# Kernel tuning notes

Hardware: AMD Instinct MI355X
Metric: run time of the kernel (lower is better)

## Reference

```python
import jax, jax.numpy as jnp
import numpy as np

# Block node counts (dst nodes are a prefix of src nodes, DGL convention)
N = [540672, 33792, 3072, 512]


def _sage_layer(h, src, dst, num_dst, W_self, W_neigh, b):
    # DGL SAGEConv with 'mean' aggregator:
    #   out = h_dst @ W_self + mean_{u in N(v)} h_u @ W_neigh + b
    msgs = h[src]  # [E, F] ragged gather
    agg = jax.ops.segment_sum(msgs, dst, num_segments=num_dst)
    deg = jax.ops.segment_sum(jnp.ones(dst.shape, h.dtype), dst, num_segments=num_dst)
    mean = agg / jnp.maximum(deg, 1.0)[:, None]
    return h[:num_dst] @ W_self + mean @ W_neigh + b


def setup_inputs() -> dict:
    key = jax.random.key(0)
    ks = jax.random.split(key, 16)
    E = [506880, 30720, 2560]
    in_feats, n_hidden, n_classes = 256, 1024, 47
    sc = lambda f: 1.0 / np.sqrt(f)
    return {
        "x": jax.random.normal(ks[0], (N[0], in_feats), jnp.float32),
        "src0": jax.random.randint(ks[1], (E[0],), 0, N[0]),
        "dst0": jax.random.randint(ks[2], (E[0],), 0, N[1]),
        "src1": jax.random.randint(ks[3], (E[1],), 0, N[1]),
        "dst1": jax.random.randint(ks[4], (E[1],), 0, N[2]),
        "src2": jax.random.randint(ks[5], (E[2],), 0, N[2]),
        "dst2": jax.random.randint(ks[6], (E[2],), 0, N[3]),
        "W_self0": jax.random.normal(ks[7], (in_feats, n_hidden), jnp.float32) * sc(in_feats),
        "W_neigh0": jax.random.normal(ks[8], (in_feats, n_hidden), jnp.float32) * sc(in_feats),
        "b0": jnp.zeros((n_hidden,), jnp.float32),
        "W_self1": jax.random.normal(ks[9], (n_hidden, n_hidden), jnp.float32) * sc(n_hidden),
        "W_neigh1": jax.random.normal(ks[10], (n_hidden, n_hidden), jnp.float32) * sc(n_hidden),
        "b1": jnp.zeros((n_hidden,), jnp.float32),
        "W_self2": jax.random.normal(ks[11], (n_hidden, n_classes), jnp.float32) * sc(n_hidden),
        "W_neigh2": jax.random.normal(ks[12], (n_hidden, n_classes), jnp.float32) * sc(n_hidden),
        "b2": jnp.zeros((n_classes,), jnp.float32),
    }


def reference(x, src0, dst0, src1, dst1, src2, dst2,
              W_self0, W_neigh0, b0, W_self1, W_neigh1, b1,
              W_self2, W_neigh2, b2):
    # Layer 0: [N0, in] -> [N1, hidden], ReLU (dropout omitted: eval mode)
    h = _sage_layer(x, src0, dst0, N[1], W_self0, W_neigh0, b0)
    h = jax.nn.relu(h)
    # Layer 1: [N1, hidden] -> [N2, hidden], ReLU
    h = _sage_layer(h, src1, dst1, N[2], W_self1, W_neigh1, b1)
    h = jax.nn.relu(h)
    # Layer 2: [N2, hidden] -> [N3, classes], no activation
    h = _sage_layer(h, src2, dst2, N[3], W_self2, W_neigh2, b2)
    return h
```

## Files before the change

kernel.cpp:

```cpp
#include <hip/hip_runtime.h>

#define E0 506880
#define E1 30720
#define E2 2560
#define NN0 540672
#define NN1 33792
#define NN2 3072
#define NN3 512
#define F_IN 256
#define F_HID 1024
#define F_OUT 47

typedef __attribute__((ext_vector_type(8))) short short8;
typedef __attribute__((ext_vector_type(4))) float f32x4;

__device__ __forceinline__ float bf_lo(unsigned int u) {
    return __uint_as_float(u << 16);
}
__device__ __forceinline__ float bf_hi(unsigned int u) {
    return __uint_as_float(u & 0xFFFF0000u);
}
__device__ __forceinline__ unsigned short f2bf(float f) {
    unsigned int u = __float_as_uint(f);
    u = (u + 0x7FFFu + ((u >> 16) & 1u)) >> 16;
    return (unsigned short)u;
}
__device__ __forceinline__ unsigned int pack2(float a, float b) {
    return (unsigned int)f2bf(a) | ((unsigned int)f2bf(b) << 16);
}

__global__ __launch_bounds__(256) void count_dst(
    const int* __restrict__ dst, int* __restrict__ cnt, int E)
{
    int i = blockIdx.x * blockDim.x + threadIdx.x;
    if (i < E) atomicAdd(&cnt[dst[i]], 1);
}

__global__ __launch_bounds__(1024) void scan_excl(
    const int* __restrict__ cnt, int* __restrict__ cursor, int n)
{
    __shared__ int part[1024];
    int t = threadIdx.x;
    int per = (n + 1023) >> 10;
    int lo = t * per;
    int hi = min(n, lo + per);
    int s = 0;
    for (int i = lo; i < hi; ++i) s += cnt[i];
    part[t] = s;
    __syncthreads();
    for (int d = 1; d < 1024; d <<= 1) {
        int v = part[t];
        int add = (t >= d) ? part[t - d] : 0;
        __syncthreads();
        part[t] = v + add;
        __syncthreads();
    }
    int off = (t == 0) ? 0 : part[t - 1];
    for (int i = lo; i < hi; ++i) { cursor[i] = off; off += cnt[i]; }
}

__global__ __launch_bounds__(256) void fill_adj(
    const int* __restrict__ src, const int* __restrict__ dst,
    int* __restrict__ cursor, int* __restrict__ adj, int E)
{
    int i = blockIdx.x * blockDim.x + threadIdx.x;
    if (i < E) {
        int pos = atomicAdd(&cursor[dst[i]], 1);
        adj[pos] = src[i];
    }
}

__global__ __launch_bounds__(256) void cast_f32_bf16(
    const float* __restrict__ in, unsigned short* __restrict__ out, int n8)
{
    int i = blockIdx.x * blockDim.x + threadIdx.x;
    if (i >= n8) return;
    float4 a = *(const float4*)(in + (size_t)i * 8);
    float4 b = *(const float4*)(in + (size_t)i * 8 + 4);
    uint4 o;
    o.x = pack2(a.x, a.y); o.y = pack2(a.z, a.w);
    o.z = pack2(b.x, b.y); o.w = pack2(b.z, b.w);
    *(uint4*)(out + (size_t)i * 8) = o;
}

__global__ __launch_bounds__(256) void transpose_cast(
    const float* __restrict__ W, unsigned short* __restrict__ Wt, int K, int N)
{
    __shared__ float t[32][33];
    int k0 = blockIdx.x * 32;
    int n0 = blockIdx.y * 32;
    int tx = threadIdx.x & 31;
    int ty = threadIdx.x >> 5;
    #pragma unroll
    for (int i = 0; i < 4; ++i) {
        int r = ty * 4 + i;
        t[r][tx] = W[(size_t)(k0 + r) * N + n0 + tx];
    }
    __syncthreads();
    #pragma unroll
    for (int i = 0; i < 4; ++i) {
        int nr = ty * 4 + i;
        Wt[(size_t)(n0 + nr) * K + k0 + tx] = f2bf(t[tx][nr]);
    }
}

__global__ __launch_bounds__(256) void gather_mean_f32(
    const float* __restrict__ feat, const int* __restrict__ adj,
    const int* __restrict__ cnt, const int* __restrict__ cur,
    unsigned short* __restrict__ agg, int num_dst)
{
    int wave = (blockIdx.x * blockDim.x + threadIdx.x) >> 6;
    int lane = threadIdx.x & 63;
    if (wave >= num_dst) return;
    int d = cnt[wave];
    int start = cur[wave] - d;
    float4 a0 = make_float4(0.f, 0.f, 0.f, 0.f), a1 = a0, a2 = a0, a3 = a0;
    int j = 0;
    for (; j + 3 < d; j += 4) {
        int i0 = adj[start + j + 0], i1 = adj[start + j + 1];
        int i2 = adj[start + j + 2], i3 = adj[start + j + 3];
        float4 v0 = *(const float4*)(feat + (size_t)i0 * F_IN + lane * 4);
        float4 v1 = *(const float4*)(feat + (size_t)i1 * F_IN + lane * 4);
        float4 v2 = *(const float4*)(feat + (size_t)i2 * F_IN + lane * 4);
        float4 v3 = *(const float4*)(feat + (size_t)i3 * F_IN + lane * 4);
        a0.x += v0.x; a0.y += v0.y; a0.z += v0.z; a0.w += v0.w;
        a1.x += v1.x; a1.y += v1.y; a1.z += v1.z; a1.w += v1.w;
        a2.x += v2.x; a2.y += v2.y; a2.z += v2.z; a2.w += v2.w;
        a3.x += v3.x; a3.y += v3.y; a3.z += v3.z; a3.w += v3.w;
    }
    for (; j < d; ++j) {
        int i0 = adj[start + j];
        float4 v0 = *(const float4*)(feat + (size_t)i0 * F_IN + lane * 4);
        a0.x += v0.x; a0.y += v0.y; a0.z += v0.z; a0.w += v0.w;
    }
    float inv = 1.0f / (float)(d > 0 ? d : 1);
    float sx = (a0.x + a1.x) + (a2.x + a3.x);
    float sy = (a0.y + a1.y) + (a2.y + a3.y);
    float sz = (a0.z + a1.z) + (a2.z + a3.z);
    float sw = (a0.w + a1.w) + (a2.w + a3.w);
    uint2 o;
    o.x = pack2(sx * inv, sy * inv);
    o.y = pack2(sz * inv, sw * inv);
    *(uint2*)(agg + (size_t)wave * F_IN + lane * 4) = o;
}

__global__ __launch_bounds__(256) void gather_mean_bf16(
    const unsigned short* __restrict__ feat, const int* __restrict__ adj,
    const int* __restrict__ cnt, const int* __restrict__ cur,
    unsigned short* __restrict__ agg, int num_dst)
{
    int wave = (blockIdx.x * blockDim.x + threadIdx.x) >> 6;
    int lane = threadIdx.x & 63;
    if (wave >= num_dst) return;
    int d = cnt[wave];
    int start = cur[wave] - d;
    float acc[16];
    #pragma unroll
    for (int c = 0; c < 16; ++c) acc[c] = 0.f;
    int j = 0;
    for (; j + 1 < d; j += 2) {
        const unsigned short* f0 = feat + (size_t)adj[start + j] * F_HID + lane * 16;
        const unsigned short* f1 = feat + (size_t)adj[start + j + 1] * F_HID + lane * 16;
        uint4 p0 = *(const uint4*)f0;
        uint4 p1 = *(const uint4*)(f0 + 8);
        uint4 q0 = *(const uint4*)f1;
        uint4 q1 = *(const uint4*)(f1 + 8);
        acc[0] += bf_lo(p0.x); acc[1] += bf_hi(p0.x);
        acc[2] += bf_lo(p0.y); acc[3] += bf_hi(p0.y);
        acc[4] += bf_lo(p0.z); acc[5] += bf_hi(p0.z);
        acc[6] += bf_lo(p0.w); acc[7] += bf_hi(p0.w);
        acc[8]  += bf_lo(p1.x); acc[9]  += bf_hi(p1.x);
        acc[10] += bf_lo(p1.y); acc[11] += bf_hi(p1.y);
        acc[12] += bf_lo(p1.z); acc[13] += bf_hi(p1.z);
        acc[14] += bf_lo(p1.w); acc[15] += bf_hi(p1.w);
        acc[0] += bf_lo(q0.x); acc[1] += bf_hi(q0.x);
        acc[2] += bf_lo(q0.y); acc[3] += bf_hi(q0.y);
        acc[4] += bf_lo(q0.z); acc[5] += bf_hi(q0.z);
        acc[6] += bf_lo(q0.w); acc[7] += bf_hi(q0.w);
        acc[8]  += bf_lo(q1.x); acc[9]  += bf_hi(q1.x);
        acc[10] += bf_lo(q1.y); acc[11] += bf_hi(q1.y);
        acc[12] += bf_lo(q1.z); acc[13] += bf_hi(q1.z);
        acc[14] += bf_lo(q1.w); acc[15] += bf_hi(q1.w);
    }
    if (j < d) {
        const unsigned short* f0 = feat + (size_t)adj[start + j] * F_HID + lane * 16;
        uint4 p0 = *(const uint4*)f0;
        uint4 p1 = *(const uint4*)(f0 + 8);
        acc[0] += bf_lo(p0.x); acc[1] += bf_hi(p0.x);
        acc[2] += bf_lo(p0.y); acc[3] += bf_hi(p0.y);
        acc[4] += bf_lo(p0.z); acc[5] += bf_hi(p0.z);
        acc[6] += bf_lo(p0.w); acc[7] += bf_hi(p0.w);
        acc[8]  += bf_lo(p1.x); acc[9]  += bf_hi(p1.x);
        acc[10] += bf_lo(p1.y); acc[11] += bf_hi(p1.y);
        acc[12] += bf_lo(p1.z); acc[13] += bf_hi(p1.z);
        acc[14] += bf_lo(p1.w); acc[15] += bf_hi(p1.w);
    }
    float inv = 1.0f / (float)(d > 0 ? d : 1);
    uint4 o0, o1;
    o0.x = pack2(acc[0] * inv, acc[1] * inv);
    o0.y = pack2(acc[2] * inv, acc[3] * inv);
    o0.z = pack2(acc[4] * inv, acc[5] * inv);
    o0.w = pack2(acc[6] * inv, acc[7] * inv);
    o1.x = pack2(acc[8] * inv, acc[9] * inv);
    o1.y = pack2(acc[10] * inv, acc[11] * inv);
    o1.z = pack2(acc[12] * inv, acc[13] * inv);
    o1.w = pack2(acc[14] * inv, acc[15] * inv);
    unsigned short* ap = agg + (size_t)wave * F_HID + lane * 16;
    *(uint4*)ap = o0;
    *(uint4*)(ap + 8) = o1;
}

__global__ __launch_bounds__(256, 2) void sage_mfma_gemm(
    const unsigned short* __restrict__ A1, const unsigned short* __restrict__ A2,
    const unsigned short* __restrict__ Wt1, const unsigned short* __restrict__ Wt2,
    const float* __restrict__ bias, unsigned short* __restrict__ C,
    int M, int N, int K, int relu)
{
    __shared__ __align__(16) unsigned short As[128 * 40];
    __shared__ __align__(16) unsigned short Bs[128 * 40];

    const int tid  = threadIdx.x;
    const int wave = tid >> 6;
    const int lane = tid & 63;
    const int wy = wave >> 1, wx = wave & 1;
    const int quad = lane >> 4, l16 = lane & 15;
    const int col0 = blockIdx.x * 128;
    const int row0 = blockIdx.y * 128;

    f32x4 acc[4][4];
    #pragma unroll
    for (int i = 0; i < 4; ++i)
        #pragma unroll
        for (int j = 0; j < 4; ++j)
            acc[i][j] = (f32x4){0.f, 0.f, 0.f, 0.f};

    for (int pass = 0; pass < 2; ++pass) {
        const unsigned short* A  = pass ? A2  : A1;
        const unsigned short* Wt = pass ? Wt2 : Wt1;
        for (int k0 = 0; k0 < K; k0 += 32) {
            #pragma unroll
            for (int q = 0; q < 2; ++q) {
                int f = tid + q * 256;
                int r = f >> 2, kq = (f & 3) * 8;
                float4 v = *(const float4*)(A + (size_t)(row0 + r) * K + k0 + kq);
                *(float4*)(&As[r * 40 + kq]) = v;
            }
            #pragma unroll
            for (int q = 0; q < 2; ++q) {
                int f = tid + q * 256;
                int n = f >> 2, kq = (f & 3) * 8;
                float4 v = *(const float4*)(Wt + (size_t)(col0 + n) * K + k0 + kq);
                *(float4*)(&Bs[n * 40 + kq]) = v;
            }
            __syncthreads();
            short8 af[4], bfr[4];
            #pragma unroll
            for (int mi = 0; mi < 4; ++mi)
                af[mi] = *(const short8*)(&As[(wy * 64 + mi * 16 + l16) * 40 + quad * 8]);
            #pragma unroll
            for (int ni = 0; ni < 4; ++ni)
                bfr[ni] = *(const short8*)(&Bs[(wx * 64 + ni * 16 + l16) * 40 + quad * 8]);
            #pragma unroll
            for (int mi = 0; mi < 4; ++mi)
                #pragma unroll
                for (int ni = 0; ni < 4; ++ni)
                    acc[mi][ni] = __builtin_amdgcn_mfma_f32_16x16x32_bf16(
                        af[mi], bfr[ni], acc[mi][ni], 0, 0, 0);
            __syncthreads();
        }
    }

    #pragma unroll
    for (int ni = 0; ni < 4; ++ni) {
        int col = col0 + wx * 64 + ni * 16 + l16;
        float bc = bias[col];
        #pragma unroll
        for (int mi = 0; mi < 4; ++mi) {
            int row = row0 + wy * 64 + mi * 16 + quad * 4;
            #pragma unroll
            for (int r = 0; r < 4; ++r) {
                float v = acc[mi][ni][r] + bc;
                if (relu) v = fmaxf(v, 0.0f);
                C[(size_t)(row + r) * N + col] = f2bf(v);
            }
        }
    }
}

__global__ __launch_bounds__(256) void skinny_gemm_blk(
    const unsigned short* __restrict__ A1, const unsigned short* __restrict__ A2,
    const float* __restrict__ W1, const float* __restrict__ W2,
    const float* __restrict__ bias, float* __restrict__ C, int K)
{
    __shared__ float red[4][64];
    int m = blockIdx.x;
    int wave = threadIdx.x >> 6;
    int lane = threadIdx.x & 63;
    const unsigned short* a1 = A1 + (size_t)m * K;
    const unsigned short* a2 = A2 + (size_t)m * K;
    float acc = 0.f;
    if (lane < F_OUT) {
        int kb = wave * (K >> 2), ke = kb + (K >> 2);
        #pragma unroll 8
        for (int k = kb; k < ke; ++k) {
            acc = fmaf(bf_lo((unsigned int)a1[k]), W1[(size_t)k * F_OUT + lane], acc);
            acc = fmaf(bf_lo((unsigned int)a2[k]), W2[(size_t)k * F_OUT + lane], acc);
        }
    }
    red[wave][lane] = acc;
    __syncthreads();
    if (wave == 0 && lane < F_OUT) {
        float v = (red[0][lane] + red[1][lane]) + (red[2][lane] + red[3][lane])
                + bias[lane];
        C[(size_t)m * F_OUT + lane] = v;
    }
}

extern "C" void kernel_launch(void* const* d_in, const int* in_sizes, int n_in,
                              void* d_out, int out_size, void* d_ws, size_t ws_size,
                              hipStream_t stream)
{
    const float* x   = (const float*)d_in[0];
    const int* src0  = (const int*)d_in[1];
    const int* dst0  = (const int*)d_in[2];
    const int* src1  = (const int*)d_in[3];
    const int* dst1  = (const int*)d_in[4];
    const int* src2  = (const int*)d_in[5];
    const int* dst2  = (const int*)d_in[6];
    const float* Wself0  = (const float*)d_in[7];
    const float* Wneigh0 = (const float*)d_in[8];
    const float* b0      = (const float*)d_in[9];
    const float* Wself1  = (const float*)d_in[10];
    const float* Wneigh1 = (const float*)d_in[11];
    const float* b1      = (const float*)d_in[12];
    const float* Wself2  = (const float*)d_in[13];
    const float* Wneigh2 = (const float*)d_in[14];
    const float* b2      = (const float*)d_in[15];
    float* out = (float*)d_out;

    char* base = (char*)d_ws;
    auto alloc = [&](size_t bytes) -> char* {
        char* p = base;
        base += (bytes + 255) & ~(size_t)255;
        return p;
    };
    unsigned short* h0   = (unsigned short*)alloc((size_t)NN1 * F_HID * 2);
    unsigned short* h1   = (unsigned short*)alloc((size_t)NN2 * F_HID * 2);
    unsigned short* agg0 = (unsigned short*)alloc((size_t)NN1 * F_IN * 2);
    unsigned short* agg1 = (unsigned short*)alloc((size_t)NN2 * F_HID * 2);
    unsigned short* agg2 = (unsigned short*)alloc((size_t)NN3 * F_HID * 2);
    unsigned short* xbf  = (unsigned short*)alloc((size_t)NN1 * F_IN * 2);
    unsigned short* Wt0s = (unsigned short*)alloc((size_t)F_HID * F_IN * 2);
    unsigned short* Wt0n = (unsigned short*)alloc((size_t)F_HID * F_IN * 2);
    unsigned short* Wt1s = (unsigned short*)alloc((size_t)F_HID * F_HID * 2);
    unsigned short* Wt1n = (unsigned short*)alloc((size_t)F_HID * F_HID * 2);
    int* cnt0 = (int*)alloc((size_t)(NN1 + NN2 + NN3) * 4);
    int* cnt1 = cnt0 + NN1;
    int* cnt2 = cnt1 + NN2;
    int* cur0 = (int*)alloc((size_t)NN1 * 4);
    int* cur1 = (int*)alloc((size_t)NN2 * 4);
    int* cur2 = (int*)alloc((size_t)NN3 * 4);
    int* adj0 = (int*)alloc((size_t)E0 * 4);
    int* adj1 = (int*)alloc((size_t)E1 * 4);
    int* adj2 = (int*)alloc((size_t)E2 * 4);

    hipMemsetAsync(cnt0, 0, (size_t)(NN1 + NN2 + NN3) * 4, stream);

    int n8 = NN1 * F_IN / 8;
    cast_f32_bf16<<<dim3((n8 + 255) / 256), dim3(256), 0, stream>>>(x, xbf, n8);
    transpose_cast<<<dim3(F_IN / 32, F_HID / 32), dim3(256), 0, stream>>>(
        Wself0, Wt0s, F_IN, F_HID);
    transpose_cast<<<dim3(F_IN / 32, F_HID / 32), dim3(256), 0, stream>>>(
        Wneigh0, Wt0n, F_IN, F_HID);
    transpose_cast<<<dim3(F_HID / 32, F_HID / 32), dim3(256), 0, stream>>>(
        Wself1, Wt1s, F_HID, F_HID);
    transpose_cast<<<dim3(F_HID / 32, F_HID / 32), dim3(256), 0, stream>>>(
        Wneigh1, Wt1n, F_HID, F_HID);

    count_dst<<<dim3((E0 + 255) / 256), dim3(256), 0, stream>>>(dst0, cnt0, E0);
    count_dst<<<dim3((E1 + 255) / 256), dim3(256), 0, stream>>>(dst1, cnt1, E1);
    count_dst<<<dim3((E2 + 255) / 256), dim3(256), 0, stream>>>(dst2, cnt2, E2);
    scan_excl<<<dim3(1), dim3(1024), 0, stream>>>(cnt0, cur0, NN1);
    scan_excl<<<dim3(1), dim3(1024), 0, stream>>>(cnt1, cur1, NN2);
    scan_excl<<<dim3(1), dim3(1024), 0, stream>>>(cnt2, cur2, NN3);
    fill_adj<<<dim3((E0 + 255) / 256), dim3(256), 0, stream>>>(src0, dst0, cur0, adj0, E0);
    fill_adj<<<dim3((E1 + 255) / 256), dim3(256), 0, stream>>>(src1, dst1, cur1, adj1, E1);
    fill_adj<<<dim3((E2 + 255) / 256), dim3(256), 0, stream>>>(src2, dst2, cur2, adj2, E2);

    gather_mean_f32<<<dim3(NN1 / 4), dim3(256), 0, stream>>>(
        x, adj0, cnt0, cur0, agg0, NN1);
    sage_mfma_gemm<<<dim3(F_HID / 128, NN1 / 128), dim3(256), 0, stream>>>(
        xbf, agg0, Wt0s, Wt0n, b0, h0, NN1, F_HID, F_IN, 1);

    gather_mean_bf16<<<dim3(NN2 / 4), dim3(256), 0, stream>>>(
        h0, adj1, cnt1, cur1, agg1, NN2);
    sage_mfma_gemm<<<dim3(F_HID / 128, NN2 / 128), dim3(256), 0, stream>>>(
        h0, agg1, Wt1s, Wt1n, b1, h1, NN2, F_HID, F_HID, 1);

    gather_mean_bf16<<<dim3(NN3 / 4), dim3(256), 0, stream>>>(
        h1, adj2, cnt2, cur2, agg2, NN3);
    skinny_gemm_blk<<<dim3(NN3), dim3(256), 0, stream>>>(
        h1, agg2, Wself2, Wneigh2, b2, out, F_HID);
}
```

Measured before the change: 1.007 ms.

## Merge preprocessing launches and load GEMM tiles directly into LDS

The four weight transpose-casts, three degree counts, three scans and three adjacency fills each collapse into a single launch that picks its work by block or global index, cutting launch overhead and idle gaps. The MFMA GEMM now stages A and B tiles with global_load_lds (direct global-to-LDS copies) in place of register round-trips, which means dropping the 40-element padded LDS row stride for an unpadded 32. That removes VGPR staging but may add LDS bank conflicts on the fragment reads.

```diff
diff --git a/kernel.cpp b/kernel.cpp
--- a/kernel.cpp
+++ b/kernel.cpp
@@ -14,6 +14,13 @@
 typedef __attribute__((ext_vector_type(8))) short short8;
 typedef __attribute__((ext_vector_type(4))) float f32x4;
 
+typedef __attribute__((address_space(1))) const unsigned int as1_u32;
+typedef __attribute__((address_space(3))) unsigned int as3_u32;
+
+__device__ __forceinline__ void gload16(const unsigned short* g, unsigned short* l) {
+    __builtin_amdgcn_global_load_lds((as1_u32*)g, (as3_u32*)l, 16, 0, 0);
+}
+
 __device__ __forceinline__ float bf_lo(unsigned int u) {
     return __uint_as_float(u << 16);
 }
@@ -29,17 +36,26 @@
     return (unsigned int)f2bf(a) | ((unsigned int)f2bf(b) << 16);
 }
 
-__global__ __launch_bounds__(256) void count_dst(
-    const int* __restrict__ dst, int* __restrict__ cnt, int E)
+__global__ __launch_bounds__(256) void count_dst3(
+    const int* __restrict__ d0, const int* __restrict__ d1, const int* __restrict__ d2,
+    int* __restrict__ cnt0, int* __restrict__ cnt1, int* __restrict__ cnt2)
 {
     int i = blockIdx.x * blockDim.x + threadIdx.x;
-    if (i < E) atomicAdd(&cnt[dst[i]], 1);
-}
-
-__global__ __launch_bounds__(1024) void scan_excl(
-    const int* __restrict__ cnt, int* __restrict__ cursor, int n)
+    if (i < E0)                 atomicAdd(&cnt0[d0[i]], 1);
+    else if (i < E0 + E1)       atomicAdd(&cnt1[d1[i - E0]], 1);
+    else if (i < E0 + E1 + E2)  atomicAdd(&cnt2[d2[i - E0 - E1]], 1);
+}
+
+__global__ __launch_bounds__(1024) void scan_excl3(
+    const int* __restrict__ c0, int* __restrict__ u0,
+    const int* __restrict__ c1, int* __restrict__ u1,
+    const int* __restrict__ c2, int* __restrict__ u2)
 {
     __shared__ int part[1024];
+    const int* cnt; int* cursor; int n;
+    if (blockIdx.x == 0)      { cnt = c0; cursor = u0; n = NN1; }
+    else if (blockIdx.x == 1) { cnt = c1; cursor = u1; n = NN2; }
+    else                      { cnt = c2; cursor = u2; n = NN3; }
     int t = threadIdx.x;
     int per = (n + 1023) >> 10;
     int lo = t * per;
@@ -59,14 +75,25 @@
     for (int i = lo; i < hi; ++i) { cursor[i] = off; off += cnt[i]; }
 }
 
-__global__ __launch_bounds__(256) void fill_adj(
-    const int* __restrict__ src, const int* __restrict__ dst,
-    int* __restrict__ cursor, int* __restrict__ adj, int E)
+__global__ __launch_bounds__(256) void fill_adj3(
+    const int* __restrict__ s0, const int* __restrict__ d0,
+    const int* __restrict__ s1, const int* __restrict__ d1,
+    const int* __restrict__ s2, const int* __restrict__ d2,
+    int* __restrict__ u0, int* __restrict__ u1, int* __restrict__ u2,
+    int* __restrict__ a0, int* __restrict__ a1, int* __restrict__ a2)
 {
     int i = blockIdx.x * blockDim.x + threadIdx.x;
-    if (i < E) {
-        int pos = atomicAdd(&cursor[dst[i]], 1);
-        adj[pos] = src[i];
+    if (i < E0) {
+        int pos = atomicAdd(&u0[d0[i]], 1);
+        a0[pos] = s0[i];
+    } else if (i < E0 + E1) {
+        int j = i - E0;
+        int pos = atomicAdd(&u1[d1[j]], 1);
+        a1[pos] = s1[j];
+    } else if (i < E0 + E1 + E2) {
+        int j = i - E0 - E1;
+        int pos = atomicAdd(&u2[d2[j]], 1);
+        a2[pos] = s2[j];
     }
 }
 
@@ -83,12 +110,23 @@
     *(uint4*)(out + (size_t)i * 8) = o;
 }
 
-__global__ __launch_bounds__(256) void transpose_cast(
-    const float* __restrict__ W, unsigned short* __restrict__ Wt, int K, int N)
+__global__ __launch_bounds__(256) void transpose_cast4(
+    const float* __restrict__ Ws0, unsigned short* __restrict__ Ts0,
+    const float* __restrict__ Wn0, unsigned short* __restrict__ Tn0,
+    const float* __restrict__ Ws1, unsigned short* __restrict__ Ts1,
+    const float* __restrict__ Wn1, unsigned short* __restrict__ Tn1)
 {
     __shared__ float t[32][33];
-    int k0 = blockIdx.x * 32;
-    int n0 = blockIdx.y * 32;
+    int b = blockIdx.x;
+    const float* W; unsigned short* T; int K, tt;
+    if (b < 256)       { W = Ws0; T = Ts0; K = F_IN;  tt = b; }
+    else if (b < 512)  { W = Wn0; T = Tn0; K = F_IN;  tt = b - 256; }
+    else if (b < 1536) { W = Ws1; T = Ts1; K = F_HID; tt = b - 512; }
+    else               { W = Wn1; T = Tn1; K = F_HID; tt = b - 1536; }
+    const int N = F_HID;
+    int ktiles = K >> 5;
+    int k0 = (tt % ktiles) * 32;
+    int n0 = (tt / ktiles) * 32;
     int tx = threadIdx.x & 31;
     int ty = threadIdx.x >> 5;
     #pragma unroll
@@ -100,7 +138,7 @@
     #pragma unroll
     for (int i = 0; i < 4; ++i) {
         int nr = ty * 4 + i;
-        Wt[(size_t)(n0 + nr) * K + k0 + tx] = f2bf(t[tx][nr]);
+        T[(size_t)(n0 + nr) * K + k0 + tx] = f2bf(t[tx][nr]);
     }
 }
 
@@ -216,8 +254,8 @@
     const float* __restrict__ bias, unsigned short* __restrict__ C,
     int M, int N, int K, int relu)
 {
-    __shared__ __align__(16) unsigned short As[128 * 40];
-    __shared__ __align__(16) unsigned short Bs[128 * 40];
+    __shared__ __align__(16) unsigned short As[128 * 32];
+    __shared__ __align__(16) unsigned short Bs[128 * 32];
 
     const int tid  = threadIdx.x;
     const int wave = tid >> 6;
@@ -227,6 +265,15 @@
     const int col0 = blockIdx.x * 128;
     const int row0 = blockIdx.y * 128;
 
+    const int c0  = wave * 64 + lane;
+    const int r0  = c0 >> 2, kq0 = (c0 & 3) * 8;
+    const int c1  = c0 + 256;
+    const int r1  = c1 >> 2, kq1 = (c1 & 3) * 8;
+    unsigned short* ldsA0 = &As[(size_t)wave * 512];
+    unsigned short* ldsA1 = &As[2048 + (size_t)wave * 512];
+    unsigned short* ldsB0 = &Bs[(size_t)wave * 512];
+    unsigned short* ldsB1 = &Bs[2048 + (size_t)wave * 512];
+
     f32x4 acc[4][4];
     #pragma unroll
     for (int i = 0; i < 4; ++i)
@@ -237,29 +284,23 @@
     for (int pass = 0; pass < 2; ++pass) {
         const unsigned short* A  = pass ? A2  : A1;
         const unsigned short* Wt = pass ? Wt2 : Wt1;
+        const unsigned short* gA0 = A  + (size_t)(row0 + r0) * K + kq0;
+        const unsigned short* gA1 = A  + (size_t)(row0 + r1) * K + kq1;
+        const unsigned short* gB0 = Wt + (size_t)(col0 + r0) * K + kq0;
+        const unsigned short* gB1 = Wt + (size_t)(col0 + r1) * K + kq1;
         for (int k0 = 0; k0 < K; k0 += 32) {
-            #pragma unroll
-            for (int q = 0; q < 2; ++q) {
-                int f = tid + q * 256;
-                int r = f >> 2, kq = (f & 3) * 8;
-                float4 v = *(const float4*)(A + (size_t)(row0 + r) * K + k0 + kq);
-                *(float4*)(&As[r * 40 + kq]) = v;
-            }
-            #pragma unroll
-            for (int q = 0; q < 2; ++q) {
-                int f = tid + q * 256;
-                int n = f >> 2, kq = (f & 3) * 8;
-                float4 v = *(const float4*)(Wt + (size_t)(col0 + n) * K + k0 + kq);
-                *(float4*)(&Bs[n * 40 + kq]) = v;
-            }
+            gload16(gA0 + k0, ldsA0);
+            gload16(gA1 + k0, ldsA1);
+            gload16(gB0 + k0, ldsB0);
+            gload16(gB1 + k0, ldsB1);
             __syncthreads();
             short8 af[4], bfr[4];
             #pragma unroll
             for (int mi = 0; mi < 4; ++mi)
-                af[mi] = *(const short8*)(&As[(wy * 64 + mi * 16 + l16) * 40 + quad * 8]);
+                af[mi] = *(const short8*)(&As[(wy * 64 + mi * 16 + l16) * 32 + quad * 8]);
             #pragma unroll
             for (int ni = 0; ni < 4; ++ni)
-                bfr[ni] = *(const short8*)(&Bs[(wx * 64 + ni * 16 + l16) * 40 + quad * 8]);
+                bfr[ni] = *(const short8*)(&Bs[(wx * 64 + ni * 16 + l16) * 32 + quad * 8]);
             #pragma unroll
             for (int mi = 0; mi < 4; ++mi)
                 #pragma unroll
@@ -368,24 +409,16 @@
 
     int n8 = NN1 * F_IN / 8;
     cast_f32_bf16<<<dim3((n8 + 255) / 256), dim3(256), 0, stream>>>(x, xbf, n8);
-    transpose_cast<<<dim3(F_IN / 32, F_HID / 32), dim3(256), 0, stream>>>(
-        Wself0, Wt0s, F_IN, F_HID);
-    transpose_cast<<<dim3(F_IN / 32, F_HID / 32), dim3(256), 0, stream>>>(
-        Wneigh0, Wt0n, F_IN, F_HID);
-    transpose_cast<<<dim3(F_HID / 32, F_HID / 32), dim3(256), 0, stream>>>(
-        Wself1, Wt1s, F_HID, F_HID);
-    transpose_cast<<<dim3(F_HID / 32, F_HID / 32), dim3(256), 0, stream>>>(
-        Wneigh1, Wt1n, F_HID, F_HID);
-
-    count_dst<<<dim3((E0 + 255) / 256), dim3(256), 0, stream>>>(dst0, cnt0, E0);
-    count_dst<<<dim3((E1 + 255) / 256), dim3(256), 0, stream>>>(dst1, cnt1, E1);
-    count_dst<<<dim3((E2 + 255) / 256), dim3(256), 0, stream>>>(dst2, cnt2, E2);
-    scan_excl<<<dim3(1), dim3(1024), 0, stream>>>(cnt0, cur0, NN1);
-    scan_excl<<<dim3(1), dim3(1024), 0, stream>>>(cnt1, cur1, NN2);
-    scan_excl<<<dim3(1), dim3(1024), 0, stream>>>(cnt2, cur2, NN3);
-    fill_adj<<<dim3((E0 + 255) / 256), dim3(256), 0, stream>>>(src0, dst0, cur0, adj0, E0);
-    fill_adj<<<dim3((E1 + 255) / 256), dim3(256), 0, stream>>>(src1, dst1, cur1, adj1, E1);
-    fill_adj<<<dim3((E2 + 255) / 256), dim3(256), 0, stream>>>(src2, dst2, cur2, adj2, E2);
+    transpose_cast4<<<dim3(2560), dim3(256), 0, stream>>>(
+        Wself0, Wt0s, Wneigh0, Wt0n, Wself1, Wt1s, Wneigh1, Wt1n);
+
+    const int ET = E0 + E1 + E2;
+    count_dst3<<<dim3((ET + 255) / 256), dim3(256), 0, stream>>>(
+        dst0, dst1, dst2, cnt0, cnt1, cnt2);
+    scan_excl3<<<dim3(3), dim3(1024), 0, stream>>>(
+        cnt0, cur0, cnt1, cur1, cnt2, cur2);
+    fill_adj3<<<dim3((ET + 255) / 256), dim3(256), 0, stream>>>(
+        src0, dst0, src1, dst1, src2, dst2, cur0, cur1, cur2, adj0, adj1, adj2);
 
     gather_mean_f32<<<dim3(NN1 / 4), dim3(256), 0, stream>>>(
         x, adj0, cnt0, cur0, agg0, NN1);
```

Result: faster. 977.9 us (-2.9%).
